# Kernel optimization log

Hardware: AMD Instinct MI355X
Metric: run time of the kernel (lower is better)

Reference implementation:

```python
import jax, jax.numpy as jnp
import numpy as np

CELL_DIM = 64
FIELD_SIZE = 1.0

def setup_inputs() -> dict:
    key = jax.random.key(0)
    k1, k2 = jax.random.split(key)
    x = jax.random.normal(k1, (8192, CELL_DIM), dtype=jnp.float32)
    placeCells = jax.random.normal(k2, (512, CELL_DIM), dtype=jnp.float32)
    return {"x": x, "placeCells": placeCells}

def reference(x, placeCells):
    # states: (N, cellDim)
    states = x.reshape(-1, CELL_DIM)
    # broadcast L1 distance to every codebook cell: (N, numCells)
    l1 = jnp.sum(jnp.abs(states[:, None, :] - placeCells[None, :, :]), axis=-1)
    dists_squared = l1 * l1
    unnormalized = -dists_squared / (2.0 * FIELD_SIZE * FIELD_SIZE)
    return jax.nn.softmax(unnormalized, axis=1)
```

## Files before the change

### kernel.cpp

```cpp
#include <hip/hip_runtime.h>

#define DIM    64
#define NCELLS 512
#define ROWS_PER_BLOCK 32
#define NROWS  8192
#define NBLOCKS (NROWS / ROWS_PER_BLOCK)
#define PCT_FLOATS (DIM * NCELLS)
#define XT_FLOATS  (ROWS_PER_BLOCK * DIM)
#define LDS_BYTES  ((PCT_FLOATS + XT_FLOATS) * 4)

__global__ __launch_bounds__(1024, 4)
void placecells_kernel(const float* __restrict__ x,
                       const float* __restrict__ pc,
                       float* __restrict__ out)
{
    extern __shared__ float lds[];
    float* pcT = lds;
    float* xT  = lds + PCT_FLOATS;

    const int tid = (int)threadIdx.x;
    const int l   = tid & 63;
    const int w   = __builtin_amdgcn_readfirstlane(tid >> 6);
    const int rowBase = (int)blockIdx.x * ROWS_PER_BLOCK + w * 2;

    {
        float2 v = *(const float2*)(x + (size_t)blockIdx.x * ROWS_PER_BLOCK * DIM + 2 * tid);
        *(float2*)(&xT[2 * tid]) = v;
    }

    auto pc_ld = [&](int i) -> float4 {
        int idx = i * 1024 + tid;
        int cl  = idx >> 4;
        int kq  = idx & 15;
        return *(const float4*)(pc + cl * DIM + kq * 4);
    };
    auto pc_st = [&](int i, float4 v) {
        int idx = i * 1024 + tid;
        int cl  = idx >> 4;
        int kq  = idx & 15;
        int pq  = (cl >> 2) ^ kq;
        float* p = &pcT[(kq * 4) * NCELLS + pq * 4 + (cl & 3)];
        p[0 * NCELLS] = v.x;
        p[1 * NCELLS] = v.y;
        p[2 * NCELLS] = v.z;
        p[3 * NCELLS] = v.w;
    };
    float4 s0 = pc_ld(0), s1 = pc_ld(1), s2 = pc_ld(2), s3 = pc_ld(3);
    float4 s4 = pc_ld(4), s5 = pc_ld(5), s6 = pc_ld(6), s7 = pc_ld(7);
    pc_st(0, s0); pc_st(1, s1); pc_st(2, s2); pc_st(3, s3);
    pc_st(4, s4); pc_st(5, s5); pc_st(6, s6); pc_st(7, s7);

    __syncthreads();

    float4 a0A{0,0,0,0}, a0B{0,0,0,0};
    float4 a1A{0,0,0,0}, a1B{0,0,0,0};

    const float* xr0 = &xT[(w * 2 + 0) * DIM];
    const float* xr1 = &xT[(w * 2 + 1) * DIM];

    #pragma unroll
    for (int k4 = 0; k4 < 16; ++k4) {
        float4 xv0 = *(const float4*)(xr0 + k4 * 4);
        float4 xv1 = *(const float4*)(xr1 + k4 * 4);
        const int pqA = (l ^ k4) * 4;
        #pragma unroll
        for (int j = 0; j < 4; ++j) {
            const float* rowp = &pcT[(k4 * 4 + j) * NCELLS];
            float4 pvA = *(const float4*)(rowp + pqA);
            float4 pvB = *(const float4*)(rowp + pqA + 256);
            float x0 = (j == 0) ? xv0.x : (j == 1) ? xv0.y : (j == 2) ? xv0.z : xv0.w;
            float x1 = (j == 0) ? xv1.x : (j == 1) ? xv1.y : (j == 2) ? xv1.z : xv1.w;
            a0A.x += fabsf(x0 - pvA.x); a0A.y += fabsf(x0 - pvA.y);
            a0A.z += fabsf(x0 - pvA.z); a0A.w += fabsf(x0 - pvA.w);
            a0B.x += fabsf(x0 - pvB.x); a0B.y += fabsf(x0 - pvB.y);
            a0B.z += fabsf(x0 - pvB.z); a0B.w += fabsf(x0 - pvB.w);
            a1A.x += fabsf(x1 - pvA.x); a1A.y += fabsf(x1 - pvA.y);
            a1A.z += fabsf(x1 - pvA.z); a1A.w += fabsf(x1 - pvA.w);
            a1B.x += fabsf(x1 - pvB.x); a1B.y += fabsf(x1 - pvB.y);
            a1B.z += fabsf(x1 - pvB.z); a1B.w += fabsf(x1 - pvB.w);
        }
    }

    {
        float mn0 = fminf(fminf(fminf(a0A.x, a0A.y), fminf(a0A.z, a0A.w)),
                          fminf(fminf(a0B.x, a0B.y), fminf(a0B.z, a0B.w)));
        float mn1 = fminf(fminf(fminf(a1A.x, a1A.y), fminf(a1A.z, a1A.w)),
                          fminf(fminf(a1B.x, a1B.y), fminf(a1B.z, a1B.w)));
        #pragma unroll
        for (int off = 32; off > 0; off >>= 1) {
            mn0 = fminf(mn0, __shfl_xor(mn0, off, 64));
            mn1 = fminf(mn1, __shfl_xor(mn1, off, 64));
        }
        float m20 = mn0 * mn0;
        float m21 = mn1 * mn1;

        float e00 = __expf(0.5f * (m20 - a0A.x * a0A.x));
        float e01 = __expf(0.5f * (m20 - a0A.y * a0A.y));
        float e02 = __expf(0.5f * (m20 - a0A.z * a0A.z));
        float e03 = __expf(0.5f * (m20 - a0A.w * a0A.w));
        float e04 = __expf(0.5f * (m20 - a0B.x * a0B.x));
        float e05 = __expf(0.5f * (m20 - a0B.y * a0B.y));
        float e06 = __expf(0.5f * (m20 - a0B.z * a0B.z));
        float e07 = __expf(0.5f * (m20 - a0B.w * a0B.w));
        float e10 = __expf(0.5f * (m21 - a1A.x * a1A.x));
        float e11 = __expf(0.5f * (m21 - a1A.y * a1A.y));
        float e12 = __expf(0.5f * (m21 - a1A.z * a1A.z));
        float e13 = __expf(0.5f * (m21 - a1A.w * a1A.w));
        float e14 = __expf(0.5f * (m21 - a1B.x * a1B.x));
        float e15 = __expf(0.5f * (m21 - a1B.y * a1B.y));
        float e16 = __expf(0.5f * (m21 - a1B.z * a1B.z));
        float e17 = __expf(0.5f * (m21 - a1B.w * a1B.w));

        float sum0 = ((e00 + e01) + (e02 + e03)) + ((e04 + e05) + (e06 + e07));
        float sum1 = ((e10 + e11) + (e12 + e13)) + ((e14 + e15) + (e16 + e17));
        #pragma unroll
        for (int off = 32; off > 0; off >>= 1) {
            sum0 += __shfl_xor(sum0, off, 64);
            sum1 += __shfl_xor(sum1, off, 64);
        }
        float inv0 = 1.0f / sum0;
        float inv1 = 1.0f / sum1;

        float* orow0 = out + (size_t)(rowBase + 0) * NCELLS;
        float* orow1 = out + (size_t)(rowBase + 1) * NCELLS;
        *(float4*)(orow0 + 4 * l)       = make_float4(e00 * inv0, e01 * inv0, e02 * inv0, e03 * inv0);
        *(float4*)(orow0 + 256 + 4 * l) = make_float4(e04 * inv0, e05 * inv0, e06 * inv0, e07 * inv0);
        *(float4*)(orow1 + 4 * l)       = make_float4(e10 * inv1, e11 * inv1, e12 * inv1, e13 * inv1);
        *(float4*)(orow1 + 256 + 4 * l) = make_float4(e14 * inv1, e15 * inv1, e16 * inv1, e17 * inv1);
    }
}

extern "C" void kernel_launch(void* const* d_in, const int* in_sizes, int n_in,
                              void* d_out, int out_size, void* d_ws, size_t ws_size,
                              hipStream_t stream)
{
    const float* x  = (const float*)d_in[0];
    const float* pc = (const float*)d_in[1];
    float* out = (float*)d_out;
    placecells_kernel<<<dim3(NBLOCKS), dim3(1024), LDS_BYTES, stream>>>(x, pc, out);
}
```

Measured before the change: 71.98 us.

## Split codebook staging into two K-halves to overlap LDS fill with compute

```diff
diff --git a/kernel.cpp b/kernel.cpp
--- a/kernel.cpp
+++ b/kernel.cpp
@@ -2,12 +2,13 @@
 
 #define DIM    64
 #define NCELLS 512
+#define KHALF  32
 #define ROWS_PER_BLOCK 32
 #define NROWS  8192
 #define NBLOCKS (NROWS / ROWS_PER_BLOCK)
-#define PCT_FLOATS (DIM * NCELLS)
+#define PCH_FLOATS (KHALF * NCELLS)
 #define XT_FLOATS  (ROWS_PER_BLOCK * DIM)
-#define LDS_BYTES  ((PCT_FLOATS + XT_FLOATS) * 4)
+#define LDS_BYTES  ((2 * PCH_FLOATS + XT_FLOATS) * 4)
 
 __global__ __launch_bounds__(1024, 4)
 void placecells_kernel(const float* __restrict__ x,
@@ -15,42 +16,47 @@
                        float* __restrict__ out)
 {
     extern __shared__ float lds[];
-    float* pcT = lds;
-    float* xT  = lds + PCT_FLOATS;
+    float* pcH0 = lds;
+    float* pcH1 = lds + PCH_FLOATS;
+    float* xT   = lds + 2 * PCH_FLOATS;
 
     const int tid = (int)threadIdx.x;
     const int l   = tid & 63;
     const int w   = __builtin_amdgcn_readfirstlane(tid >> 6);
     const int rowBase = (int)blockIdx.x * ROWS_PER_BLOCK + w * 2;
 
-    {
-        float2 v = *(const float2*)(x + (size_t)blockIdx.x * ROWS_PER_BLOCK * DIM + 2 * tid);
-        *(float2*)(&xT[2 * tid]) = v;
-    }
-
-    auto pc_ld = [&](int i) -> float4 {
+    auto pc_ld = [&](int h, int i) -> float4 {
         int idx = i * 1024 + tid;
-        int cl  = idx >> 4;
-        int kq  = idx & 15;
-        return *(const float4*)(pc + cl * DIM + kq * 4);
+        int cl  = idx >> 3;
+        int kq  = idx & 7;
+        return *(const float4*)(pc + cl * DIM + h * KHALF + kq * 4);
     };
-    auto pc_st = [&](int i, float4 v) {
+    auto pc_st = [&](float* buf, int h, int i, float4 v) {
         int idx = i * 1024 + tid;
-        int cl  = idx >> 4;
-        int kq  = idx & 15;
-        int pq  = (cl >> 2) ^ kq;
-        float* p = &pcT[(kq * 4) * NCELLS + pq * 4 + (cl & 3)];
+        int cl  = idx >> 3;
+        int kq  = idx & 7;
+        int k4g = h * 8 + kq;
+        int pq  = (cl >> 2) ^ k4g;
+        float* p = &buf[(kq * 4) * NCELLS + pq * 4 + (cl & 3)];
         p[0 * NCELLS] = v.x;
         p[1 * NCELLS] = v.y;
         p[2 * NCELLS] = v.z;
         p[3 * NCELLS] = v.w;
     };
-    float4 s0 = pc_ld(0), s1 = pc_ld(1), s2 = pc_ld(2), s3 = pc_ld(3);
-    float4 s4 = pc_ld(4), s5 = pc_ld(5), s6 = pc_ld(6), s7 = pc_ld(7);
-    pc_st(0, s0); pc_st(1, s1); pc_st(2, s2); pc_st(3, s3);
-    pc_st(4, s4); pc_st(5, s5); pc_st(6, s6); pc_st(7, s7);
+
+    float4 t0 = pc_ld(0,0), t1 = pc_ld(0,1), t2 = pc_ld(0,2), t3 = pc_ld(0,3);
+    float4 u0 = pc_ld(1,0), u1 = pc_ld(1,1), u2 = pc_ld(1,2), u3 = pc_ld(1,3);
+    {
+        float2 v = *(const float2*)(x + (size_t)blockIdx.x * ROWS_PER_BLOCK * DIM + 2 * tid);
+        *(float2*)(&xT[2 * tid]) = v;
+    }
+    pc_st(pcH0, 0, 0, t0); pc_st(pcH0, 0, 1, t1);
+    pc_st(pcH0, 0, 2, t2); pc_st(pcH0, 0, 3, t3);
 
     __syncthreads();
+
+    pc_st(pcH1, 1, 0, u0); pc_st(pcH1, 1, 1, u1);
+    pc_st(pcH1, 1, 2, u2); pc_st(pcH1, 1, 3, u3);
 
     float4 a0A{0,0,0,0}, a0B{0,0,0,0};
     float4 a1A{0,0,0,0}, a1B{0,0,0,0};
@@ -58,28 +64,37 @@
     const float* xr0 = &xT[(w * 2 + 0) * DIM];
     const float* xr1 = &xT[(w * 2 + 1) * DIM];
 
-    #pragma unroll
-    for (int k4 = 0; k4 < 16; ++k4) {
-        float4 xv0 = *(const float4*)(xr0 + k4 * 4);
-        float4 xv1 = *(const float4*)(xr1 + k4 * 4);
-        const int pqA = (l ^ k4) * 4;
+    auto compute_half = [&](const float* buf, int h) {
         #pragma unroll
-        for (int j = 0; j < 4; ++j) {
-            const float* rowp = &pcT[(k4 * 4 + j) * NCELLS];
-            float4 pvA = *(const float4*)(rowp + pqA);
-            float4 pvB = *(const float4*)(rowp + pqA + 256);
-            float x0 = (j == 0) ? xv0.x : (j == 1) ? xv0.y : (j == 2) ? xv0.z : xv0.w;
-            float x1 = (j == 0) ? xv1.x : (j == 1) ? xv1.y : (j == 2) ? xv1.z : xv1.w;
-            a0A.x += fabsf(x0 - pvA.x); a0A.y += fabsf(x0 - pvA.y);
-            a0A.z += fabsf(x0 - pvA.z); a0A.w += fabsf(x0 - pvA.w);
-            a0B.x += fabsf(x0 - pvB.x); a0B.y += fabsf(x0 - pvB.y);
-            a0B.z += fabsf(x0 - pvB.z); a0B.w += fabsf(x0 - pvB.w);
-            a1A.x += fabsf(x1 - pvA.x); a1A.y += fabsf(x1 - pvA.y);
-            a1A.z += fabsf(x1 - pvA.z); a1A.w += fabsf(x1 - pvA.w);
-            a1B.x += fabsf(x1 - pvB.x); a1B.y += fabsf(x1 - pvB.y);
-            a1B.z += fabsf(x1 - pvB.z); a1B.w += fabsf(x1 - pvB.w);
+        for (int kq = 0; kq < 8; ++kq) {
+            const int k4g = h * 8 + kq;
+            float4 xv0 = *(const float4*)(xr0 + h * KHALF + kq * 4);
+            float4 xv1 = *(const float4*)(xr1 + h * KHALF + kq * 4);
+            const int pqA = (l ^ k4g) * 4;
+            #pragma unroll
+            for (int j = 0; j < 4; ++j) {
+                const float* rowp = &buf[(kq * 4 + j) * NCELLS];
+                float4 pvA = *(const float4*)(rowp + pqA);
+                float4 pvB = *(const float4*)(rowp + pqA + 256);
+                float x0 = (j == 0) ? xv0.x : (j == 1) ? xv0.y : (j == 2) ? xv0.z : xv0.w;
+                float x1 = (j == 0) ? xv1.x : (j == 1) ? xv1.y : (j == 2) ? xv1.z : xv1.w;
+                a0A.x += fabsf(x0 - pvA.x); a0A.y += fabsf(x0 - pvA.y);
+                a0A.z += fabsf(x0 - pvA.z); a0A.w += fabsf(x0 - pvA.w);
+                a0B.x += fabsf(x0 - pvB.x); a0B.y += fabsf(x0 - pvB.y);
+                a0B.z += fabsf(x0 - pvB.z); a0B.w += fabsf(x0 - pvB.w);
+                a1A.x += fabsf(x1 - pvA.x); a1A.y += fabsf(x1 - pvA.y);
+                a1A.z += fabsf(x1 - pvA.z); a1A.w += fabsf(x1 - pvA.w);
+                a1B.x += fabsf(x1 - pvB.x); a1B.y += fabsf(x1 - pvB.y);
+                a1B.z += fabsf(x1 - pvB.z); a1B.w += fabsf(x1 - pvB.w);
+            }
         }
-    }
+    };
+
+    compute_half(pcH0, 0);
+
+    __syncthreads();
+
+    compute_half(pcH1, 1);
 
     {
         float mn0 = fminf(fminf(fminf(a0A.x, a0A.y), fminf(a0A.z, a0A.w)),
```

After: 72.64 us. No clear change (+0.9%).
